# Optimization experiments

Measured on AMD Instinct MI355X. Metric: run time of the kernel, lower is better.

Reference implementation:

```python
import jax, jax.numpy as jnp
import numpy as np

NA, NPA, NT = 4096, 8192, 4096  # authors, papers, terms
HEADS = 8

def _ln(x, g, b):
    m = jnp.mean(x, -1, keepdims=True)
    v = jnp.var(x, -1, keepdims=True)
    return (x - m) * jax.lax.rsqrt(v + 1e-5) * g + b

def _gat(x_src, x_dst, src, dst, W, a_s, a_d, b, n_dst):
    # PyG-style GATConv (shared lin for src/dst, no self loops), per edge type.
    heads, outc = a_s.shape
    h_s = (x_src @ W).reshape(-1, heads, outc)
    h_d = (x_dst @ W).reshape(-1, heads, outc)
    e = jax.nn.leaky_relu(jnp.sum(h_s * a_s, -1)[src] + jnp.sum(h_d * a_d, -1)[dst], 0.2)  # [E,H]
    m = jax.ops.segment_max(e, dst, num_segments=n_dst)
    m = jnp.where(jnp.isfinite(m), m, 0.0)
    w = jnp.exp(e - m[dst])
    den = jax.ops.segment_sum(w, dst, num_segments=n_dst)
    alpha = w / (den[dst] + 1e-16)
    out = jax.ops.segment_sum(h_s[src] * alpha[..., None], dst, num_segments=n_dst)
    return out.reshape(n_dst, heads * outc) + b

def _gtl(x, peQ, peK, db, Wq, bq, Wk, bk, Wv, bv, Wo, bo, g1, be1, Wf1, bf1, Wf2, bf2, g2, be2):
    # PE-modulated dense multi-head attention + FFN, pre/post LN residual blocks.
    N, D = x.shape
    dh = D // HEADS
    Q = (x @ Wq + bq + peQ).reshape(N, HEADS, dh)
    K = (x @ Wk + bk + peK).reshape(N, HEADS, dh)
    V = (x @ Wv + bv).reshape(N, HEADS, dh)
    s = jnp.einsum('nhd,mhd->hnm', Q, K) / jnp.sqrt(jnp.float32(dh)) + db[None, None, :]
    o = jnp.einsum('hnm,mhd->nhd', jax.nn.softmax(s, -1), V).reshape(N, D) @ Wo + bo
    x = _ln(x + o, g1, be1)
    f = jax.nn.relu(x @ Wf1 + bf1) @ Wf2 + bf2
    return _ln(x + f, g2, be2)

def _forward(F, I):
    (x_author, x_paper, x_term, original_A, t1_W, t1_b, t2_W, t2_b, t3_W, t3_b,
     gat1_W, gat1_as, gat1_ad, gat1_b, gat2_W, gat2_as, gat2_ad, gat2_b,
     pe_embed, peWQ, peWK,
     gt_Wq, gt_bq, gt_Wk, gt_bk, gt_Wv, gt_bv, gt_Wo, gt_bo,
     gt_g1, gt_be1, gt_Wf1, gt_bf1, gt_Wf2, gt_bf2, gt_g2, gt_be2,
     cat_W, cat_b, mlp_W1, mlp_b1, mlp_W2, mlp_b2) = F
    (ap_src, ap_dst, pa_src, pa_dst, pt_src, pt_dst, tp_src, tp_dst, deg) = I
    xa = jax.nn.relu(x_author @ t1_W + t1_b)
    xp = jax.nn.relu(x_paper @ t2_W + t2_b)
    xt = jax.nn.relu(x_term @ t3_W + t3_b)
    # to_hetero GAT layer 1 (heads=8, out=128): sum over incoming edge types, relu
    h_p1 = jax.nn.relu(_gat(xa, xp, ap_src, ap_dst, gat1_W[0], gat1_as[0], gat1_ad[0], gat1_b[0], NPA)
                       + _gat(xt, xp, tp_src, tp_dst, gat1_W[3], gat1_as[3], gat1_ad[3], gat1_b[3], NPA))
    h_a1 = jax.nn.relu(_gat(xp, xa, pa_src, pa_dst, gat1_W[1], gat1_as[1], gat1_ad[1], gat1_b[1], NA))
    # layer 2 (heads=1); only author output feeds the graph transformer
    h_a2 = _gat(h_p1, h_a1, pa_src, pa_dst, gat2_W[1], gat2_as[1], gat2_ad[1], gat2_b[1], NA)
    # learned positional encodings + adjacency reconstruction loss
    peQ = pe_embed @ peWQ
    peK = pe_embed @ peWK
    S = jax.nn.sigmoid(peQ @ peK.T)  # [NA, NA]
    loss_pe = jnp.mean((S[None] - original_A) ** 2)
    db = jnp.log(jnp.maximum(deg.astype(jnp.float32), 1.0))  # degree key bias
    x = h_a2
    outs = [x]
    for i in range(gt_Wq.shape[0]):
        x = _gtl(x, peQ, peK, db, gt_Wq[i], gt_bq[i], gt_Wk[i], gt_bk[i], gt_Wv[i], gt_bv[i],
                 gt_Wo[i], gt_bo[i], gt_g1[i], gt_be1[i], gt_Wf1[i], gt_bf1[i], gt_Wf2[i], gt_bf2[i],
                 gt_g2[i], gt_be2[i])
        outs.append(x)
    x_gt = jax.nn.relu(jnp.concatenate(outs, -1) @ cat_W + cat_b)
    logits = jax.nn.relu(x_gt @ mlp_W1 + mlp_b1) @ mlp_W2 + mlp_b2
    return loss_pe, jax.nn.softmax(logits, -1), x_gt

def setup_inputs() -> dict:
    key = jax.random.key(0)
    ks = iter(jax.random.split(key, 100))
    def rn(sh, s=1.0):
        return jax.random.normal(next(ks), sh, jnp.float32) * s
    def ri(sh, hi, lo=0):
        return jax.random.randint(next(ks), sh, lo, hi)
    d = {}
    d['x_author'] = rn((NA, 334)); d['x_paper'] = rn((NPA, 512)); d['x_term'] = rn((NT, 128))
    d['ap_src'] = ri((80000,), NA); d['ap_dst'] = ri((80000,), NPA)
    d['pa_src'] = ri((80000,), NPA); d['pa_dst'] = ri((80000,), NA)
    d['pt_src'] = ri((160000,), NPA); d['pt_dst'] = ri((160000,), NT)
    d['tp_src'] = ri((160000,), NT); d['tp_dst'] = ri((160000,), NPA)
    d['original_A'] = (jax.random.uniform(next(ks), (4, NA, NA)) < 0.005).astype(jnp.float32)
    d['deg'] = ri((NA,), 64, 1)
    p = 0.05
    d['t1_W'] = rn((334, 128), p); d['t1_b'] = jnp.zeros((128,))
    d['t2_W'] = rn((512, 128), p); d['t2_b'] = jnp.zeros((128,))
    d['t3_W'] = rn((128, 128), p); d['t3_b'] = jnp.zeros((128,))
    d['gat1_W'] = rn((4, 128, 1024), p); d['gat1_as'] = rn((4, 8, 128), p)
    d['gat1_ad'] = rn((4, 8, 128), p); d['gat1_b'] = jnp.zeros((4, 1024))
    d['gat2_W'] = rn((4, 1024, 128), p); d['gat2_as'] = rn((4, 1, 128), p)
    d['gat2_ad'] = rn((4, 1, 128), p); d['gat2_b'] = jnp.zeros((4, 128))
    d['pe_embed'] = rn((NA, 128), p); d['peWQ'] = rn((128, 128), p); d['peWK'] = rn((128, 128), p)
    d['gt_Wq'] = rn((2, 128, 128), p); d['gt_bq'] = jnp.zeros((2, 128))
    d['gt_Wk'] = rn((2, 128, 128), p); d['gt_bk'] = jnp.zeros((2, 128))
    d['gt_Wv'] = rn((2, 128, 128), p); d['gt_bv'] = jnp.zeros((2, 128))
    d['gt_Wo'] = rn((2, 128, 128), p); d['gt_bo'] = jnp.zeros((2, 128))
    d['gt_g1'] = jnp.ones((2, 128)); d['gt_be1'] = jnp.zeros((2, 128))
    d['gt_Wf1'] = rn((2, 128, 256), p); d['gt_bf1'] = jnp.zeros((2, 256))
    d['gt_Wf2'] = rn((2, 256, 128), p); d['gt_bf2'] = jnp.zeros((2, 128))
    d['gt_g2'] = jnp.ones((2, 128)); d['gt_be2'] = jnp.zeros((2, 128))
    d['cat_W'] = rn((384, 128), p); d['cat_b'] = jnp.zeros((128,))
    d['mlp_W1'] = rn((128, 256), p); d['mlp_b1'] = jnp.zeros((256,))
    d['mlp_W2'] = rn((256, 4), p); d['mlp_b2'] = jnp.zeros((4,))
    return d

def reference(x_author, x_paper, x_term, ap_src, ap_dst, pa_src, pa_dst, pt_src, pt_dst, tp_src, tp_dst, original_A, deg, t1_W, t1_b, t2_W, t2_b, t3_W, t3_b, gat1_W, gat1_as, gat1_ad, gat1_b, gat2_W, gat2_as, gat2_ad, gat2_b, pe_embed, peWQ, peWK, gt_Wq, gt_bq, gt_Wk, gt_bk, gt_Wv, gt_bv, gt_Wo, gt_bo, gt_g1, gt_be1, gt_Wf1, gt_bf1, gt_Wf2, gt_bf2, gt_g2, gt_be2, cat_W, cat_b, mlp_W1, mlp_b1, mlp_W2, mlp_b2):
    F = (x_author, x_paper, x_term, original_A, t1_W, t1_b, t2_W, t2_b, t3_W, t3_b,
         gat1_W, gat1_as, gat1_ad, gat1_b, gat2_W, gat2_as, gat2_ad, gat2_b,
         pe_embed, peWQ, peWK,
         gt_Wq, gt_bq, gt_Wk, gt_bk, gt_Wv, gt_bv, gt_Wo, gt_bo,
         gt_g1, gt_be1, gt_Wf1, gt_bf1, gt_Wf2, gt_bf2, gt_g2, gt_be2,
         cat_W, cat_b, mlp_W1, mlp_b1, mlp_W2, mlp_b2)
    I = (ap_src, ap_dst, pa_src, pa_dst, pt_src, pt_dst, tp_src, tp_dst, deg)
    return _forward(F, I)
```

## Files before the change

kernel.cpp:

```cpp
#include <hip/hip_runtime.h>
#include <math.h>

#define NA   4096
#define NPA  8192
#define NT   4096
#define E_AP 80000
#define E_PA 80000
#define E_TP 160000
#define E_TOT (E_AP + E_TP + E_PA)
#define NSLOT (NPA + NPA + NA)
#define ASPLIT 4

typedef __attribute__((ext_vector_type(4))) float f32x4;
typedef __attribute__((ext_vector_type(8))) short s16x8;
typedef __attribute__((ext_vector_type(8))) unsigned short u16x8;
typedef unsigned short ushort_t;

__device__ __forceinline__ ushort_t f2bf(float f){
  unsigned u = __float_as_uint(f);
  unsigned r = u + 0x7fffu + ((u >> 16) & 1u);
  return (ushort_t)(r >> 16);
}
__device__ __forceinline__ float bf2f(ushort_t u){
  return __uint_as_float(((unsigned)u) << 16);
// ... 56 lines not shown
        int gk = k0 + ks + j;
        float fv = (gk < K) ? B[(size_t)gk * ldb + bn + n] : 0.f;
        tmp[j] = f2bf(fv);
      }
      u16x8 v0, v1;
#pragma unroll
      for (int j = 0; j < 8; ++j) { v0[j] = tmp[j]; v1[j] = tmp[8 + j]; }
      *(u16x8*)&Bs[n][ks] = v0;
      *(u16x8*)&Bs[n][ks + 8] = v1;
    } else {
      int n = tid >> 2, ks = (tid & 3) * 8;
      u16x8 v;
#pragma unroll
      for (int j = 0; j < 8; ++j) {
        int gk = k0 + ks + j;
        float fv = (gk < K) ? B[(size_t)gk * ldb + bn + n] : 0.f;
        v[j] = f2bf(fv);
      }
      *(u16x8*)&Bs[n][ks] = v;
    }
    __syncthreads();
    s16x8 a_frag[2], b_frag[NJ];
#pragma unroll
    for (int i = 0; i < 2; ++i) a_frag[i] = *(s16x8*)&As[wm + i * 16 + lid][lg * 8];
#pragma unroll
    for (int j = 0; j < NJ; ++j) b_frag[j] = *(s16x8*)&Bs[wn + j * 16 + lid][lg * 8];
#pragma unroll
    for (int i = 0; i < 2; ++i)
#pragma unroll
      for (int j = 0; j < NJ; ++j)
        acc[i][j] = __builtin_amdgcn_mfma_f32_16x16x32_bf16(a_frag[i], b_frag[j], acc[i][j], 0, 0, 0);
    __syncthreads();
  }
  if constexpr (ACT == 2) {
    __shared__ float Ct[64][132];
#pragma unroll
    for (int i = 0; i < 2; ++i) {
#pragma unroll
      for (int j = 0; j < NJ; ++j) {
        int coll = wn + j * 16 + lid;
#pragma unroll
        for (int rr = 0; rr < 4; ++rr) {
          int rowl = wm + i * 16 + lg * 4 + rr;
          float v = acc[i][j][rr];
          if (bias) v += bias[coll];
          if (addmat && coll < addCols) v += addmat[(size_t)(bm + rowl) * addLd + coll];
          Ct[rowl][coll] = v;
        }
      }
    }
    __syncthreads();
    int row = tid >> 2, part = tid & 3;
    float s = 0.f, q = 0.f;
#pragma unroll
    for (int c2 = 0; c2 < 32; ++c2) {
      float v = Ct[row][part * 32 + c2];
      s += v; q += v * v;
    }
    s += __shfl_xor(s, 1); q += __shfl_xor(q, 1);
    s += __shfl_xor(s, 2); q += __shfl_xor(q, 2);
    float mean = s * (1.f / 128.f);
    float var = q * (1.f / 128.f) - mean * mean;
    float inv = rsqrtf(var + 1e-5f);
    int r = bm + row;
    float* Cf = (float*)C;
#pragma unroll
    for (int c2 = 0; c2 < 32; ++c2) {
      int c = part * 32 + c2;
      Cf[(size_t)r * ldc + c] = (Ct[row][c] - mean) * inv * lng[c] + lnb[c];
    }
  } else if constexpr (ACT == 3) {
    __shared__ float Ct[64][132];
#pragma unroll
    for (int i = 0; i < 2; ++i) {
#pragma unroll
      for (int j = 0; j < NJ; ++j) {
        int coll = wn + j * 16 + lid;
#pragma unroll
        for (int rr = 0; rr < 4; ++rr) {
          int rowl = wm + i * 16 + lg * 4 + rr;
          Ct[rowl][coll] = acc[i][j][rr];
        }
      }
    }
    __syncthreads();
    int row = tid >> 2, part = tid & 3;
    const float* vsel = (bm + row < 8192) ? lng : lnb;
    float rd = 0.f;
    ushort_t* Cu = (ushort_t*)C;
#pragma unroll
    for (int c2 = 0; c2 < 32; ++c2) {
      int c = part * 32 + c2;
      float f = Ct[row][c];
      rd = fmaf(f, vsel[c], rd);
      Cu[(size_t)(bm + row) * ldc + c] = f2bf(f);
    }
    rd += __shfl_xor(rd, 1);
    rd += __shfl_xor(rd, 2);
    if (part == 0) rdOut[bm + row] = rd;
  } else {
#pragma unroll
    for (int i = 0; i < 2; ++i) {
#pragma unroll
      for (int j = 0; j < NJ; ++j) {
// ... 106 lines not shown
      int c = bn + wn + j * 16 + lid;
#pragma unroll
      for (int rr = 0; rr < 4; ++rr) {
        int r = bm + wm + i * 16 + lg * 4 + rr;
        float v = acc[i][j][rr];
        if (bias) v += bias[c];
        if (act == 1) v = fmaxf(v, 0.f);
        if (cBf16) ((ushort_t*)C)[(size_t)r * ldc + c] = f2bf(v);
        else       ((float*)C)[(size_t)r * ldc + c] = v;
      }
    }
  }
}

__global__ void prep_k(const float* __restrict__ gat1_b, const float* __restrict__ gat1_W,
                       const float* __restrict__ Wq, const float* __restrict__ bq,
                       const float* __restrict__ Wk, const float* __restrict__ bk,
                       const float* __restrict__ Wv, const float* __restrict__ bv,
                       const float* __restrict__ peWQ, const float* __restrict__ peWK,
                       const int* __restrict__ deg,
                       const float* __restrict__ gat1_as, const float* __restrict__ gat1_ad,
                       const int* __restrict__ ap_dst, const int* __restrict__ tp_dst,
                       const int* __restrict__ pa_dst,
                       const float* __restrict__ gt_Wo, const float* __restrict__ gt_Wf1,
                       const float* __restrict__ gt_Wf2, const float* __restrict__ cat_W,
                       const float* __restrict__ mlp_W1,
                       float* __restrict__ bsum, float* __restrict__ Wqkv,
                       float* __restrict__ bqkv, float* __restrict__ peW,
                       float* __restrict__ Bstack, float* __restrict__ dbv,
                       float* __restrict__ Ps, float* __restrict__ Pd,
                       int* __restrict__ cnt,
                       ushort_t* __restrict__ Wot, ushort_t* __restrict__ Wf1t,
                       ushort_t* __restrict__ Wf2t, ushort_t* __restrict__ catt,
                       ushort_t* __restrict__ mlp1t)
{
  int idx = blockIdx.x * blockDim.x + threadIdx.x;
  if (idx < 1024) { bsum[idx] = gat1_b[idx] + gat1_b[3 * 1024 + idx]; return; }
  idx -= 1024;
  if (idx < 2 * 128 * 384) {
    int l = idx / 49152, rem = idx % 49152;
    int k = rem / 384, c = rem % 384;
    float v;
    if (c < 128)      v = Wq[(size_t)l * 16384 + k * 128 + c];
    else if (c < 256) v = Wk[(size_t)l * 16384 + k * 128 + c - 128];
    else              v = Wv[(size_t)l * 16384 + k * 128 + c - 256];
    Wqkv[(size_t)l * 49152 + k * 384 + c] = v;
    return;
  }
  idx -= 2 * 128 * 384;
  if (idx < 2 * 384) {
    int l = idx / 384, c = idx % 384;
    float v;
    if (c < 128)      v = bq[l * 128 + c];
    else if (c < 256) v = bk[l * 128 + c - 128];
    else              v = bv[l * 128 + c - 256];
    bqkv[l * 384 + c] = v;
    return;
  }
  idx -= 2 * 384;
  if (idx < 128 * 256) {
    int k = idx / 256, c = idx % 256;
    peW[k * 256 + c] = (c < 128) ? peWQ[k * 128 + c] : peWK[k * 128 + c - 128];
    return;
  }
  idx -= 128 * 256;
  if (idx < 256 * 1024) {
    int k = idx / 1024, c = idx % 1024;
// ... 27 lines not shown
    return;
  }
  idx -= E_TOT;
  if (idx < 2 * 128 * 128) {
    int l = idx / 16384, rem = idx % 16384;
    int n = rem / 128, k = rem % 128;
    Wot[idx] = f2bf(gt_Wo[(size_t)l * 16384 + k * 128 + n]);
    return;
  }
  idx -= 2 * 128 * 128;
  if (idx < 2 * 256 * 128) {
    int l = idx / 32768, rem = idx % 32768;
    int n = rem / 128, k = rem % 128;
    Wf1t[idx] = f2bf(gt_Wf1[(size_t)l * 32768 + k * 256 + n]);
    return;
  }
  idx -= 2 * 256 * 128;
  if (idx < 2 * 128 * 256) {
    int l = idx / 32768, rem = idx % 32768;
    int n = rem / 256, k = rem % 256;
    Wf2t[idx] = f2bf(gt_Wf2[(size_t)l * 32768 + k * 128 + n]);
    return;
  }
  idx -= 2 * 128 * 256;
  if (idx < 128 * 384) {
    int n = idx / 384, k = idx % 384;
    catt[idx] = f2bf(cat_W[(size_t)k * 128 + n]);
    return;
  }
  idx -= 128 * 384;
  if (idx < 256 * 128) {
    int n = idx / 128, k = idx % 128;
    mlp1t[idx] = f2bf(mlp_W1[(size_t)k * 256 + n]);
  }
}

__global__ void scatterf_k(const int* __restrict__ ap_dst, const int* __restrict__ tp_dst,
                           const int* __restrict__ pa_dst, const int* __restrict__ off,
                           int* __restrict__ cur, int* __restrict__ eidx){
  int i = blockIdx.x * blockDim.x + threadIdx.x;
  if (i >= E_TOT) return;
  int slot, local;
  if (i < E_AP)             { local = i;                 slot = ap_dst[local]; }
  else if (i < E_AP + E_TP) { local = i - E_AP;          slot = NPA + tp_dst[local]; }
  else                      { local = i - E_AP - E_TP;   slot = 2 * NPA + pa_dst[local]; }
  int p = atomicAdd(&cur[slot], 1);
  eidx[off[slot] + p] = local;
}

__global__ __launch_bounds__(1024) void exscan_k(const int* __restrict__ in, int* __restrict__ out, int n){
  __shared__ int wsum[16];
  __shared__ int carrySh;
  int t = threadIdx.x, w = t >> 6, lane = t & 63;
  if (t == 0) carrySh = 0;
  __syncthreads();
  for (int base = 0; base < n; base += 1024){
    int carry = carrySh;
    int v = (base + t < n) ? in[base + t] : 0;
    int sc = v;
#pragma unroll
    for (int o2 = 1; o2 < 64; o2 <<= 1){
      int u = __shfl_up(sc, o2);
      if (lane >= o2) sc += u;
    }
    if (lane == 63) wsum[w] = sc;
    __syncthreads();
// ... 280 lines not shown
    l = l * scale + psum;
    m = mn;

#pragma unroll
    for (int g = 0; g < 4; ++g) {
#pragma unroll
      for (int rp = 0; rp < 4; rp += 2) {
        unsigned pack = (unsigned)f2bf(p[g][rp]) | ((unsigned)f2bf(p[g][rp + 1]) << 16);
        *(unsigned*)&Pl[w][lid][16 * g + 4 * lg + rp] = pack;
      }
    }
#pragma unroll
    for (int r = 0; r < 4; ++r) o[r] *= __shfl(scale, 4 * lg + r);
#pragma unroll
    for (int kc = 0; kc < 2; ++kc) {
      s16x8 pa = *(s16x8*)&Pl[w][lid][32 * kc + 8 * lg];
      s16x8 vb = *(s16x8*)&Vt[lid][32 * kc + 8 * lg];
      o = __builtin_amdgcn_mfma_f32_16x16x32_bf16(pa, vb, o, 0, 0, 0);
    }
  }
  float* pb = part + ((size_t)(sp * 8 + h) * NA) * 18;
#pragma unroll
  for (int r = 0; r < 4; ++r) {
    int qq = qbase + 16 * w + 4 * lg + r;
    pb[(size_t)qq * 18 + lid] = o[r];
  }
  if (lg == 0) {
    int qq = qbase + 16 * w + lid;
    pb[(size_t)qq * 18 + 16] = m;
    pb[(size_t)qq * 18 + 17] = l;
  }
}

__global__ __launch_bounds__(256) void gt_tail_k(
    const float* __restrict__ part,
    const ushort_t* __restrict__ Wot, const float* __restrict__ bo,
    const float* __restrict__ xin,
    const float* __restrict__ g1, const float* __restrict__ be1,
    const ushort_t* __restrict__ Wf1t, const float* __restrict__ bf1,
    const ushort_t* __restrict__ Wf2t, const float* __restrict__ bf2,
    const float* __restrict__ g2, const float* __restrict__ be2,
    float* __restrict__ outX)
{
  __shared__ __align__(16) ushort_t Aly[16][136];
  __shared__ __align__(16) ushort_t Bs[256][40];
  __shared__ __align__(16) ushort_t F1b[16][264];
  __shared__ float X1[16][132];
  int bm = blockIdx.x * 16;
  int tid = threadIdx.x;
  int w = tid >> 6, lane = tid & 63, lg = lane >> 4, lid = lane & 15;

  {
    int row = bm + (tid >> 4);
    int seg = tid & 15;
    int kcol = seg * 8;
    int h = kcol >> 4, d0 = kcol & 15;
    float mm = -1e30f;
#pragma unroll
    for (int sp = 0; sp < ASPLIT; ++sp)
      mm = fmaxf(mm, part[((size_t)(sp * 8 + h) * NA + row) * 18 + 16]);
    float ll = 0.f, a[8];
#pragma unroll
    for (int j = 0; j < 8; ++j) a[j] = 0.f;
#pragma unroll
    for (int sp = 0; sp < ASPLIT; ++sp){
      const float* pp = part + ((size_t)(sp * 8 + h) * NA + row) * 18;
      float wq = __expf(pp[16] - mm);
      ll += pp[17] * wq;
#pragma unroll
      for (int j = 0; j < 8; ++j) a[j] = fmaf(pp[d0 + j], wq, a[j]);
    }
    float inv = 1.f / ll;
    u16x8 v;
#pragma unroll
    for (int j = 0; j < 8; ++j) v[j] = f2bf(a[j] * inv);
    *(u16x8*)&Aly[tid >> 4][kcol] = v;
  }
  __syncthreads();

  f32x4 acc1[2];
  acc1[0] = (f32x4){0.f,0.f,0.f,0.f};
  acc1[1] = (f32x4){0.f,0.f,0.f,0.f};
  for (int k0 = 0; k0 < 128; k0 += 32){
// ... 66 lines not shown
  f32x4 acc3[2];
  acc3[0] = (f32x4){0.f,0.f,0.f,0.f};
  acc3[1] = (f32x4){0.f,0.f,0.f,0.f};
  for (int k0 = 0; k0 < 256; k0 += 32){
    int n = tid >> 1, ks = (tid & 1) * 16;
    *(u16x8*)&Bs[n][ks]     = *(const u16x8*)(Wf2t + (size_t)n * 256 + k0 + ks);
    *(u16x8*)&Bs[n][ks + 8] = *(const u16x8*)(Wf2t + (size_t)n * 256 + k0 + ks + 8);
    __syncthreads();
    s16x8 af = *(s16x8*)&F1b[lid][k0 + lg * 8];
#pragma unroll
    for (int j = 0; j < 2; ++j){
      s16x8 bf = *(s16x8*)&Bs[w * 32 + j * 16 + lid][lg * 8];
      acc3[j] = __builtin_amdgcn_mfma_f32_16x16x32_bf16(af, bf, acc3[j], 0, 0, 0);
    }
    __syncthreads();
  }
#pragma unroll
  for (int j = 0; j < 2; ++j)
#pragma unroll
    for (int rr = 0; rr < 4; ++rr){
      int r = lg * 4 + rr, c = w * 32 + j * 16 + lid;
      X1[r][c] = acc3[j][rr] + bf2[c] + X1[r][c];
    }
  __syncthreads();
  {
    int r = tid >> 4, p = tid & 15;
    float s = 0.f, q = 0.f;
#pragma unroll
    for (int j = 0; j < 8; ++j){ float v = X1[r][p * 8 + j]; s += v; q += v * v; }
#pragma unroll
    for (int mk = 1; mk < 16; mk <<= 1){ s += __shfl_xor(s, mk); q += __shfl_xor(q, mk); }
    float mean = s * (1.f / 128.f), var = q * (1.f / 128.f) - mean * mean;
    float inv = rsqrtf(var + 1e-5f);
#pragma unroll
    for (int j = 0; j < 8; ++j){
      int c = p * 8 + j;
      outX[(size_t)(bm + r) * 128 + c] = (X1[r][c] - mean) * inv * g2[c] + be2[c];
    }
  }
}

__global__ __launch_bounds__(256) void head_k(
    const float* __restrict__ hA2, const float* __restrict__ o1, const float* __restrict__ o2,
    const ushort_t* __restrict__ catt, const float* __restrict__ cat_b,
    const ushort_t* __restrict__ mlp1t, const float* __restrict__ mlp_b1,
    const float* __restrict__ mlp_W2, const float* __restrict__ mlp_b2,
    const float* __restrict__ lossAcc, float* __restrict__ out)
{
  __shared__ __align__(16) ushort_t Aly[16][392];
  __shared__ __align__(16) ushort_t Bs[256][40];
  __shared__ __align__(16) ushort_t L1b[16][264];
  __shared__ float LG[16][4];
  int bm = blockIdx.x * 16;
  int tid = threadIdx.x;
  int w = tid >> 6, lane = tid & 63, lg = lane >> 4, lid = lane & 15;
  if (blockIdx.x == 0 && tid == 0) out[0] = lossAcc[0] * (1.0f / 67108864.0f);

  {
    int r = bm + (tid >> 4), seg = tid & 15;
#pragma unroll
    for (int ch = 0; ch < 3; ++ch){
      int c0 = seg * 24 + ch * 8;
      const float* src; int cc;
      if (c0 < 128)      { src = hA2; cc = c0; }
      else if (c0 < 256) { src = o1;  cc = c0 - 128; }
      else               { src = o2;  cc = c0 - 256; }
      u16x8 v;
#pragma unroll
      for (int j = 0; j < 8; ++j) v[j] = f2bf(src[(size_t)r * 128 + cc + j]);
      *(u16x8*)&Aly[tid >> 4][c0] = v;
    }
  }
  __syncthreads();

  float* xgt = out + 1 + NA * 4;
  f32x4 acc1[2];
  acc1[0] = (f32x4){0.f,0.f,0.f,0.f};
  acc1[1] = (f32x4){0.f,0.f,0.f,0.f};
  for (int k0 = 0; k0 < 384; k0 += 32){
    int n = tid >> 1, ks = (tid & 1) * 16;
    *(u16x8*)&Bs[n][ks]     = *(const u16x8*)(catt + (size_t)n * 384 + k0 + ks);
    *(u16x8*)&Bs[n][ks + 8] = *(const u16x8*)(catt + (size_t)n * 384 + k0 + ks + 8);
    __syncthreads();
    s16x8 af = *(s16x8*)&Aly[lid][k0 + lg * 8];
#pragma unroll
    for (int j = 0; j < 2; ++j){
      s16x8 bf = *(s16x8*)&Bs[w * 32 + j * 16 + lid][lg * 8];
      acc1[j] = __builtin_amdgcn_mfma_f32_16x16x32_bf16(af, bf, acc1[j], 0, 0, 0);
    }
    __syncthreads();
  }
#pragma unroll
  for (int j = 0; j < 2; ++j)
#pragma unroll
    for (int rr = 0; rr < 4; ++rr){
      int r = lg * 4 + rr, c = w * 32 + j * 16 + lid;
      float f = fmaxf(acc1[j][rr] + cat_b[c], 0.f);
      xgt[(size_t)(bm + r) * 128 + c] = f;
      Aly[r][c] = f2bf(f);
    }
  __syncthreads();

  f32x4 acc2[4];
#pragma unroll
  for (int j = 0; j < 4; ++j) acc2[j] = (f32x4){0.f,0.f,0.f,0.f};
  for (int k0 = 0; k0 < 128; k0 += 32){
#pragma unroll
    for (int q4 = 0; q4 < 4; ++q4)
      *(u16x8*)&Bs[tid][q4 * 8] = *(const u16x8*)(mlp1t + (size_t)tid * 128 + k0 + q4 * 8);
    __syncthreads();
    s16x8 af = *(s16x8*)&Aly[lid][k0 + lg * 8];
#pragma unroll
    for (int j = 0; j < 4; ++j){
      s16x8 bf = *(s16x8*)&Bs[w * 64 + j * 16 + lid][lg * 8];
      acc2[j] = __builtin_amdgcn_mfma_f32_16x16x32_bf16(af, bf, acc2[j], 0, 0, 0);
    }
    __syncthreads();
  }
#pragma unroll
  for (int j = 0; j < 4; ++j)
#pragma unroll
    for (int rr = 0; rr < 4; ++rr){
      int r = lg * 4 + rr, c = w * 64 + j * 16 + lid;
      L1b[r][c] = f2bf(fmaxf(acc2[j][rr] + mlp_b1[c], 0.f));
    }
  __syncthreads();

  {
    int r = tid >> 4, rem = tid & 15, c = rem >> 2, p = rem & 3;
    float s = 0.f;
    for (int k = p * 64; k < p * 64 + 64; ++k)
      s = fmaf(bf2f(L1b[r][k]), mlp_W2[(size_t)k * 4 + c], s);
    s += __shfl_xor(s, 1);
    s += __shfl_xor(s, 2);
    if (p == 0) LG[r][c] = s + mlp_b2[c];
  }
  __syncthreads();
  if (tid < 16){
    int r = tid;
    float l0 = LG[r][0], l1 = LG[r][1], l2 = LG[r][2], l3 = LG[r][3];
    float mx = fmaxf(fmaxf(l0, l1), fmaxf(l2, l3));
    float e0 = __expf(l0 - mx), e1 = __expf(l1 - mx), e2 = __expf(l2 - mx), e3 = __expf(l3 - mx);
    float inv = 1.f / (e0 + e1 + e2 + e3);
    float* o = out + 1 + (size_t)(bm + r) * 4;
    o[0] = e0 * inv; o[1] = e1 * inv; o[2] = e2 * inv; o[3] = e3 * inv;
  }
}

__global__ void setval_k(float* p, float v){ p[0] = v; }

extern "C" void kernel_launch(void* const* d_in, const int* in_sizes, int n_in,
                              void* d_out, int out_size, void* d_ws, size_t ws_size,
                              hipStream_t stream)
{
  (void)in_sizes; (void)n_in; (void)out_size;
  const float* x_author = (const float*)d_in[0];
  const float* x_paper  = (const float*)d_in[1];
  const float* x_term   = (const float*)d_in[2];
  const int* ap_src = (const int*)d_in[3];
  const int* ap_dst = (const int*)d_in[4];
  const int* pa_src = (const int*)d_in[5];
  const int* pa_dst = (const int*)d_in[6];
  const int* tp_src = (const int*)d_in[9];
  const int* tp_dst = (const int*)d_in[10];
  const float* original_A = (const float*)d_in[11];
  const int* deg = (const int*)d_in[12];
  const float* t1_W = (const float*)d_in[13]; const float* t1_b = (const float*)d_in[14];
  const float* t2_W = (const float*)d_in[15]; const float* t2_b = (const float*)d_in[16];
  const float* t3_W = (const float*)d_in[17]; const float* t3_b = (const float*)d_in[18];
  const float* gat1_W  = (const float*)d_in[19];
  const float* gat1_as = (const float*)d_in[20];
  const float* gat1_ad = (const float*)d_in[21];
  const float* gat1_b  = (const float*)d_in[22];
  const float* gat2_W  = (const float*)d_in[23];
  const float* gat2_as = (const float*)d_in[24];
  const float* gat2_ad = (const float*)d_in[25];
  const float* gat2_b  = (const float*)d_in[26];
  const float* pe_embed = (const float*)d_in[27];
// ... 14 lines not shown

  char* base = (char*)d_ws;
  size_t off = 0;
  auto alloc = [&](size_t nbytes) -> void* {
    void* p = base + off;
    off += (nbytes + 255) & ~(size_t)255;
    return p;
  };
  ushort_t* xa  = (ushort_t*)alloc((size_t)NA * 128 * 2);
  ushort_t* xp  = (ushort_t*)alloc((size_t)NPA * 128 * 2);
  ushort_t* xt  = (ushort_t*)alloc((size_t)NT * 128 * 2);
  ushort_t* accP = (ushort_t*)alloc((size_t)NPA * 1024 * 2);
  ushort_t* accA = (ushort_t*)alloc((size_t)NA * 1024 * 2);
  ushort_t* agg  = (ushort_t*)alloc((size_t)NSLOT * 1024 * 2);
  float* scores = (float*)alloc((size_t)36864 * 8 * 4);
  float* Ps   = (float*)alloc(3 * 1024 * 4);
  float* Pd   = (float*)alloc(3 * 1024 * 4);
  ushort_t* hs2 = (ushort_t*)alloc((size_t)NPA * 128 * 2);
  ushort_t* hd2 = (ushort_t*)alloc((size_t)NA * 128 * 2);
  float* s2sd = (float*)alloc((size_t)(NPA + NA) * 4);
  float* hA2  = (float*)alloc((size_t)NA * 128 * 4);
  float* peQK = (float*)alloc((size_t)NA * 256 * 4);
  float* dbv  = (float*)alloc((size_t)NA * 4);
  float* bsum = (float*)alloc(1024 * 4);
  float* Wqkv = (float*)alloc((size_t)2 * 128 * 384 * 4);
  float* bqkv = (float*)alloc((size_t)2 * 384 * 4);
  float* peW  = (float*)alloc((size_t)128 * 256 * 4);
  float* Bstack = (float*)alloc((size_t)256 * 1024 * 4);
  ushort_t* Wot   = (ushort_t*)alloc((size_t)2 * 128 * 128 * 2);
  ushort_t* Wf1t  = (ushort_t*)alloc((size_t)2 * 256 * 128 * 2);
  ushort_t* Wf2t  = (ushort_t*)alloc((size_t)2 * 128 * 256 * 2);
  ushort_t* catt  = (ushort_t*)alloc((size_t)128 * 384 * 2);
  ushort_t* mlp1t = (ushort_t*)alloc((size_t)256 * 128 * 2);
  ushort_t* QKVb = (ushort_t*)alloc((size_t)NA * 384 * 2);
  float* outs1= (float*)alloc((size_t)NA * 128 * 4);
  float* outs2= (float*)alloc((size_t)NA * 128 * 4);
  int*   offb = (int*)alloc((size_t)NSLOT * 4);
  int*   eidx = (int*)alloc((size_t)E_TOT * 4);
  size_t zstart = off;
  int*      cnt   = (int*)alloc((size_t)NSLOT * 4);
  int*      cur   = (int*)alloc((size_t)NSLOT * 4);
  float*    lossAcc = (float*)alloc(256);
  size_t zlen = off - zstart;

  float* part = (float*)accP;

  if (off > ws_size){
    setval_k<<<1, 1, 0, stream>>>(out, -12345.0f);
    return;
  }

  auto gemmx = [&](int act, int tn, const void* A, const void* A2, const void* A3, int aBf16,
                   const float* B, void* C, int cBf16, const float* bias,
                   const float* addmat, int addCols, int addLd,
                   const float* lng, const float* lnb, float* rdOut,
                   int M, int N, int K, int lda, int ldb, int ldc){
    dim3 g(M / 64, N / tn, 1);
    if (tn == 128) {
      if (act == 0)      gemm_mfma_k<0,128><<<g, 256, 0, stream>>>(A, A2, A3, aBf16, B, C, cBf16, bias, addmat, addCols, addLd, lng, lnb, rdOut, M, N, K, lda, ldb, ldc);
      else if (act == 1) gemm_mfma_k<1,128><<<g, 256, 0, stream>>>(A, A2, A3, aBf16, B, C, cBf16, bias, addmat, addCols, addLd, lng, lnb, rdOut, M, N, K, lda, ldb, ldc);
      else if (act == 2) gemm_mfma_k<2,128><<<g, 256, 0, stream>>>(A, A2, A3, aBf16, B, C, cBf16, bias, addmat, addCols, addLd, lng, lnb, rdOut, M, N, K, lda, ldb, ldc);
      else               gemm_mfma_k<3,128><<<g, 256, 0, stream>>>(A, A2, A3, aBf16, B, C, cBf16, bias, addmat, addCols, addLd, lng, lnb, rdOut, M, N, K, lda, ldb, ldc);
    } else {
      if (act == 0)      gemm_mfma_k<0,64><<<g, 256, 0, stream>>>(A, A2, A3, aBf16, B, C, cBf16, bias, addmat, addCols, addLd, lng, lnb, rdOut, M, N, K, lda, ldb, ldc);
      else               gemm_mfma_k<1,64><<<g, 256, 0, stream>>>(A, A2, A3, aBf16, B, C, cBf16, bias, addmat, addCols, addLd, lng, lnb, rdOut, M, N, K, lda, ldb, ldc);
    }
  };

  hipMemsetAsync(base + zstart, 0, zlen, stream);
  prep_k<<<3781, 256, 0, stream>>>(gat1_b, gat1_W, gt_Wq, gt_bq, gt_Wk, gt_bk, gt_Wv, gt_bv,
                                   peWQ, peWK, deg, gat1_as, gat1_ad, ap_dst, tp_dst, pa_dst,
                                   gt_Wo, gt_Wf1, gt_Wf2, cat_W, mlp_W1,
                                   bsum, Wqkv, bqkv, peW, Bstack, dbv, Ps, Pd, cnt,
                                   Wot, Wf1t, Wf2t, catt, mlp1t);
  {
    GDescArr da; da.nd = 4;
    da.d[0] = { x_author, nullptr, t1_W, xa, t1_b, 0, 1, 1, NA, 128, 334, 334, 128, 128, 1, 0, 0, 0, 0 };
    da.d[1] = { x_paper,  nullptr, t2_W, xp, t2_b, 0, 1, 1, NPA, 128, 512, 512, 128, 128, 1, 0, 0, 0, 128 };
    da.d[2] = { x_term,   nullptr, t3_W, xt, t3_b, 0, 1, 1, NT, 128, 128, 128, 128, 128, 1, 0, 0, 0, 384 };
    da.d[3] = { pe_embed, nullptr, peW, peQK, nullptr, 0, 0, 0, NA, 256, 128, 128, 256, 256, 1, 0, 0, 0, 512 };
    gemm_multi_k<<<768, 256, 0, stream>>>(da);
  }
  exscan_k<<<1, 1024, 0, stream>>>(cnt, offb, NSLOT);
  scatterf_k<<<(E_TOT + 255) / 256, 256, 0, stream>>>(ap_dst, tp_dst, pa_dst, offb, cur, eidx);
  scorev_k<<<9216, 256, 0, stream>>>(xa, xp, xt, Ps, Pd, scores);
  agg8ff_k<<<NSLOT / 4, 256, 0, stream>>>(eidx, offb, cnt, ap_src, tp_src, pa_src,
                                          xa, xt, xp, scores, agg);
  {
    GDescArr da; da.nd = 2;
    da.d[0] = { agg, agg + (size_t)NPA * 1024, Bstack, accP, bsum, 1, 1, 1,
                NPA, 128, 256, 1024, 1024, 1024, 8, 128, 128, 128, 0 };
    da.d[1] = { agg + (size_t)2 * NPA * 1024, nullptr, gat1_W + 131072, accA, gat1_b + 1024, 1, 1, 1,
                NA, 128, 128, 1024, 1024, 1024, 8, 128, 128, 128, 2048 };
    gemm_multi_k<<<3072, 256, 0, stream>>>(da);
  }
  gemmx(3, 128, accP, 0, 0, 1, gat2_W + 131072, hs2, 1, 0, 0, 0, 0,
        gat2_as + 128, gat2_ad + 128, s2sd, NPA + NA, 128, 1024, 1024, 128, 128);
  gat_agg1f_k<<<NA / 4, 256, 0, stream>>>(eidx, offb + 2 * NPA, cnt + 2 * NPA, pa_src, hs2, s2sd,
                                          gat2_b + 128, hA2, NA);
  loss_mfma_k<<<dim3(64, 32), 256, 0, stream>>>(peQK, peQK + 128, original_A, lossAcc);
  const float* x = hA2;
  float* louts[2] = { outs1, outs2 };
  for (int i = 0; i < 2; ++i){
    gemmx(0, 64, x, 0, 0, 0, Wqkv + (size_t)i * 49152, QKVb, 1, bqkv + i * 384, peQK, 256, 256,
          0, 0, 0, NA, 384, 128, 128, 384, 384);
    attn_mfma_k<<<dim3(NA / 64, 8, ASPLIT), 256, 0, stream>>>(QKVb, QKVb + 128, QKVb + 256, dbv, part);
    gt_tail_k<<<NA / 16, 256, 0, stream>>>(part, Wot + (size_t)i * 16384, gt_bo + i * 128, x,
                                           gt_g1 + i * 128, gt_be1 + i * 128,
                                           Wf1t + (size_t)i * 32768, gt_bf1 + i * 256,
                                           Wf2t + (size_t)i * 32768, gt_bf2 + i * 128,
                                           gt_g2 + i * 128, gt_be2 + i * 128, louts[i]);
    x = louts[i];
  }
  head_k<<<NA / 16, 256, 0, stream>>>(hA2, outs1, outs2, catt, cat_b, mlp1t, mlp_b1,
                                      mlp_W2, mlp_b2, lossAcc, out);
}
```

Before: 646.2 us.

## Fuse next-layer QKV projection and classification head into graph-transformer tail kernel

```diff
diff --git a/kernel.cpp b/kernel.cpp
--- a/kernel.cpp
+++ b/kernel.cpp
@@ -112,44 +112,7 @@
         acc[i][j] = __builtin_amdgcn_mfma_f32_16x16x32_bf16(a_frag[i], b_frag[j], acc[i][j], 0, 0, 0);
     __syncthreads();
   }
-  if constexpr (ACT == 2) {
-    __shared__ float Ct[64][132];
-#pragma unroll
-    for (int i = 0; i < 2; ++i) {
-#pragma unroll
-      for (int j = 0; j < NJ; ++j) {
-        int coll = wn + j * 16 + lid;
-#pragma unroll
-        for (int rr = 0; rr < 4; ++rr) {
-          int rowl = wm + i * 16 + lg * 4 + rr;
-          float v = acc[i][j][rr];
-          if (bias) v += bias[coll];
-          if (addmat && coll < addCols) v += addmat[(size_t)(bm + rowl) * addLd + coll];
-          Ct[rowl][coll] = v;
-        }
-      }
-    }
-    __syncthreads();
-    int row = tid >> 2, part = tid & 3;
-    float s = 0.f, q = 0.f;
-#pragma unroll
-    for (int c2 = 0; c2 < 32; ++c2) {
-      float v = Ct[row][part * 32 + c2];
-      s += v; q += v * v;
-    }
-    s += __shfl_xor(s, 1); q += __shfl_xor(q, 1);
-    s += __shfl_xor(s, 2); q += __shfl_xor(q, 2);
-    float mean = s * (1.f / 128.f);
-    float var = q * (1.f / 128.f) - mean * mean;
-    float inv = rsqrtf(var + 1e-5f);
-    int r = bm + row;
-    float* Cf = (float*)C;
-#pragma unroll
-    for (int c2 = 0; c2 < 32; ++c2) {
-      int c = part * 32 + c2;
-      Cf[(size_t)r * ldc + c] = (Ct[row][c] - mean) * inv * lng[c] + lnb[c];
-    }
-  } else if constexpr (ACT == 3) {
+  if constexpr (ACT == 3) {
     __shared__ float Ct[64][132];
 #pragma unroll
     for (int i = 0; i < 2; ++i) {
@@ -322,7 +285,7 @@
                        int* __restrict__ cnt,
                        ushort_t* __restrict__ Wot, ushort_t* __restrict__ Wf1t,
                        ushort_t* __restrict__ Wf2t, ushort_t* __restrict__ catt,
-                       ushort_t* __restrict__ mlp1t)
+                       ushort_t* __restrict__ mlp1t, ushort_t* __restrict__ Wqkvt)
 {
   int idx = blockIdx.x * blockDim.x + threadIdx.x;
   if (idx < 1024) { bsum[idx] = gat1_b[idx] + gat1_b[3 * 1024 + idx]; return; }
@@ -416,6 +379,17 @@
   if (idx < 256 * 128) {
     int n = idx / 128, k = idx % 128;
     mlp1t[idx] = f2bf(mlp_W1[(size_t)k * 256 + n]);
+    return;
+  }
+  idx -= 256 * 128;
+  if (idx < 2 * 384 * 128) {
+    int l = idx / 49152, rem = idx % 49152;
+    int n = rem / 128, k = rem % 128;
+    float v;
+    if (n < 128)      v = Wq[(size_t)l * 16384 + k * 128 + n];
+    else if (n < 256) v = Wk[(size_t)l * 16384 + k * 128 + n - 128];
+    else              v = Wv[(size_t)l * 16384 + k * 128 + n - 256];
+    Wqkvt[idx] = f2bf(v);
   }
 }
 
@@ -762,6 +736,7 @@
   }
 }
 
+template<int MODE>
 __global__ __launch_bounds__(256) void gt_tail_k(
     const float* __restrict__ part,
     const ushort_t* __restrict__ Wot, const float* __restrict__ bo,
@@ -770,15 +745,25 @@
     const ushort_t* __restrict__ Wf1t, const float* __restrict__ bf1,
     const ushort_t* __restrict__ Wf2t, const float* __restrict__ bf2,
     const float* __restrict__ g2, const float* __restrict__ be2,
-    float* __restrict__ outX)
+    float* __restrict__ outX,
+    const ushort_t* __restrict__ Wqkvt, const float* __restrict__ bqkv,
+    const float* __restrict__ peQK, ushort_t* __restrict__ QKVb,
+    const float* __restrict__ hA2, const float* __restrict__ o1,
+    const ushort_t* __restrict__ catt, const float* __restrict__ cat_b,
+    const ushort_t* __restrict__ mlp1t, const float* __restrict__ mlp_b1,
+    const float* __restrict__ mlp_W2, const float* __restrict__ mlp_b2,
+    const float* __restrict__ lossAcc, float* __restrict__ out)
 {
-  __shared__ __align__(16) ushort_t Aly[16][136];
+  constexpr int AW = (MODE == 1) ? 392 : 136;
+  __shared__ __align__(16) ushort_t Aly[16][AW];
   __shared__ __align__(16) ushort_t Bs[256][40];
   __shared__ __align__(16) ushort_t F1b[16][264];
   __shared__ float X1[16][132];
+  __shared__ float LG[16][4];
   int bm = blockIdx.x * 16;
   int tid = threadIdx.x;
   int w = tid >> 6, lane = tid & 63, lg = lane >> 4, lid = lane & 15;
+  if (MODE == 1 && blockIdx.x == 0 && tid == 0) out[0] = lossAcc[0] * (1.0f / 67108864.0f);
 
   {
     int row = bm + (tid >> 4);
@@ -911,118 +896,138 @@
     for (int mk = 1; mk < 16; mk <<= 1){ s += __shfl_xor(s, mk); q += __shfl_xor(q, mk); }
     float mean = s * (1.f / 128.f), var = q * (1.f / 128.f) - mean * mean;
     float inv = rsqrtf(var + 1e-5f);
+    u16x8 v;
 #pragma unroll
     for (int j = 0; j < 8; ++j){
       int c = p * 8 + j;
-      outX[(size_t)(bm + r) * 128 + c] = (X1[r][c] - mean) * inv * g2[c] + be2[c];
-    }
-  }
-}
-
-__global__ __launch_bounds__(256) void head_k(
-    const float* __restrict__ hA2, const float* __restrict__ o1, const float* __restrict__ o2,
-    const ushort_t* __restrict__ catt, const float* __restrict__ cat_b,
-    const ushort_t* __restrict__ mlp1t, const float* __restrict__ mlp_b1,
-    const float* __restrict__ mlp_W2, const float* __restrict__ mlp_b2,
-    const float* __restrict__ lossAcc, float* __restrict__ out)
-{
-  __shared__ __align__(16) ushort_t Aly[16][392];
-  __shared__ __align__(16) ushort_t Bs[256][40];
-  __shared__ __align__(16) ushort_t L1b[16][264];
-  __shared__ float LG[16][4];
-  int bm = blockIdx.x * 16;
-  int tid = threadIdx.x;
-  int w = tid >> 6, lane = tid & 63, lg = lane >> 4, lid = lane & 15;
-  if (blockIdx.x == 0 && tid == 0) out[0] = lossAcc[0] * (1.0f / 67108864.0f);
-
-  {
-    int r = bm + (tid >> 4), seg = tid & 15;
-#pragma unroll
-    for (int ch = 0; ch < 3; ++ch){
-      int c0 = seg * 24 + ch * 8;
-      const float* src; int cc;
-      if (c0 < 128)      { src = hA2; cc = c0; }
-      else if (c0 < 256) { src = o1;  cc = c0 - 128; }
-      else               { src = o2;  cc = c0 - 256; }
-      u16x8 v;
-#pragma unroll
-      for (int j = 0; j < 8; ++j) v[j] = f2bf(src[(size_t)r * 128 + cc + j]);
-      *(u16x8*)&Aly[tid >> 4][c0] = v;
-    }
+      float f = (X1[r][c] - mean) * inv * g2[c] + be2[c];
+      X1[r][c] = f;
+      v[j] = f2bf(f);
+      if (MODE == 0) outX[(size_t)(bm + r) * 128 + c] = f;
+    }
+    if (MODE == 0) *(u16x8*)&Aly[r][p * 8] = v;
+    else           *(u16x8*)&Aly[r][256 + p * 8] = v;
   }
   __syncthreads();
 
-  float* xgt = out + 1 + NA * 4;
-  f32x4 acc1[2];
-  acc1[0] = (f32x4){0.f,0.f,0.f,0.f};
-  acc1[1] = (f32x4){0.f,0.f,0.f,0.f};
-  for (int k0 = 0; k0 < 384; k0 += 32){
-    int n = tid >> 1, ks = (tid & 1) * 16;
-    *(u16x8*)&Bs[n][ks]     = *(const u16x8*)(catt + (size_t)n * 384 + k0 + ks);
-    *(u16x8*)&Bs[n][ks + 8] = *(const u16x8*)(catt + (size_t)n * 384 + k0 + ks + 8);
-    __syncthreads();
-    s16x8 af = *(s16x8*)&Aly[lid][k0 + lg * 8];
-#pragma unroll
-    for (int j = 0; j < 2; ++j){
-      s16x8 bf = *(s16x8*)&Bs[w * 32 + j * 16 + lid][lg * 8];
-      acc1[j] = __builtin_amdgcn_mfma_f32_16x16x32_bf16(af, bf, acc1[j], 0, 0, 0);
-    }
-    __syncthreads();
-  }
-#pragma unroll
-  for (int j = 0; j < 2; ++j)
-#pragma unroll
-    for (int rr = 0; rr < 4; ++rr){
-      int r = lg * 4 + rr, c = w * 32 + j * 16 + lid;
-      float f = fmaxf(acc1[j][rr] + cat_b[c], 0.f);
-      xgt[(size_t)(bm + r) * 128 + c] = f;
-      Aly[r][c] = f2bf(f);
-    }
-  __syncthreads();
-
-  f32x4 acc2[4];
-#pragma unroll
-  for (int j = 0; j < 4; ++j) acc2[j] = (f32x4){0.f,0.f,0.f,0.f};
-  for (int k0 = 0; k0 < 128; k0 += 32){
-#pragma unroll
-    for (int q4 = 0; q4 < 4; ++q4)
-      *(u16x8*)&Bs[tid][q4 * 8] = *(const u16x8*)(mlp1t + (size_t)tid * 128 + k0 + q4 * 8);
-    __syncthreads();
-    s16x8 af = *(s16x8*)&Aly[lid][k0 + lg * 8];
-#pragma unroll
-    for (int j = 0; j < 4; ++j){
-      s16x8 bf = *(s16x8*)&Bs[w * 64 + j * 16 + lid][lg * 8];
-      acc2[j] = __builtin_amdgcn_mfma_f32_16x16x32_bf16(af, bf, acc2[j], 0, 0, 0);
-    }
-    __syncthreads();
-  }
-#pragma unroll
-  for (int j = 0; j < 4; ++j)
-#pragma unroll
-    for (int rr = 0; rr < 4; ++rr){
-      int r = lg * 4 + rr, c = w * 64 + j * 16 + lid;
-      L1b[r][c] = f2bf(fmaxf(acc2[j][rr] + mlp_b1[c], 0.f));
-    }
-  __syncthreads();
-
-  {
-    int r = tid >> 4, rem = tid & 15, c = rem >> 2, p = rem & 3;
-    float s = 0.f;
-    for (int k = p * 64; k < p * 64 + 64; ++k)
-      s = fmaf(bf2f(L1b[r][k]), mlp_W2[(size_t)k * 4 + c], s);
-    s += __shfl_xor(s, 1);
-    s += __shfl_xor(s, 2);
-    if (p == 0) LG[r][c] = s + mlp_b2[c];
-  }
-  __syncthreads();
-  if (tid < 16){
-    int r = tid;
-    float l0 = LG[r][0], l1 = LG[r][1], l2 = LG[r][2], l3 = LG[r][3];
-    float mx = fmaxf(fmaxf(l0, l1), fmaxf(l2, l3));
-    float e0 = __expf(l0 - mx), e1 = __expf(l1 - mx), e2 = __expf(l2 - mx), e3 = __expf(l3 - mx);
-    float inv = 1.f / (e0 + e1 + e2 + e3);
-    float* o = out + 1 + (size_t)(bm + r) * 4;
-    o[0] = e0 * inv; o[1] = e1 * inv; o[2] = e2 * inv; o[3] = e3 * inv;
+  if constexpr (MODE == 0) {
+#pragma unroll
+    for (int nb = 0; nb < 2; ++nb) {
+      f32x4 acc4[3];
+#pragma unroll
+      for (int j = 0; j < 3; ++j) acc4[j] = (f32x4){0.f,0.f,0.f,0.f};
+      for (int k0 = 0; k0 < 128; k0 += 32){
+#pragma unroll
+        for (int p = 0; p < 3; ++p){
+          int idx = tid + p * 256;
+          int n = idx >> 2, seg = (idx & 3) * 8;
+          *(u16x8*)&Bs[n][seg] = *(const u16x8*)(Wqkvt + (size_t)(nb * 192 + n) * 128 + k0 + seg);
+        }
+        __syncthreads();
+        s16x8 af = *(s16x8*)&Aly[lid][k0 + lg * 8];
+#pragma unroll
+        for (int j = 0; j < 3; ++j){
+          s16x8 bf = *(s16x8*)&Bs[w * 48 + j * 16 + lid][lg * 8];
+          acc4[j] = __builtin_amdgcn_mfma_f32_16x16x32_bf16(af, bf, acc4[j], 0, 0, 0);
+        }
+        __syncthreads();
+      }
+#pragma unroll
+      for (int j = 0; j < 3; ++j)
+#pragma unroll
+        for (int rr = 0; rr < 4; ++rr){
+          int r = lg * 4 + rr, c = nb * 192 + w * 48 + j * 16 + lid;
+          float v = acc4[j][rr] + bqkv[c];
+          if (c < 256) v += peQK[(size_t)(bm + r) * 256 + c];
+          QKVb[(size_t)(bm + r) * 384 + c] = f2bf(v);
+        }
+    }
+  } else {
+    {
+      int r = bm + (tid >> 4), seg = tid & 15;
+#pragma unroll
+      for (int ch = 0; ch < 2; ++ch){
+        int c0 = seg * 16 + ch * 8;
+        const float* src; int cc;
+        if (c0 < 128) { src = hA2; cc = c0; }
+        else          { src = o1;  cc = c0 - 128; }
+        u16x8 v;
+#pragma unroll
+        for (int j = 0; j < 8; ++j) v[j] = f2bf(src[(size_t)r * 128 + cc + j]);
+        *(u16x8*)&Aly[tid >> 4][c0] = v;
+      }
+    }
+    __syncthreads();
+    float* xgt = out + 1 + NA * 4;
+    f32x4 acc1b[2];
+    acc1b[0] = (f32x4){0.f,0.f,0.f,0.f};
+    acc1b[1] = (f32x4){0.f,0.f,0.f,0.f};
+    for (int k0 = 0; k0 < 384; k0 += 32){
+      int n = tid >> 1, ks = (tid & 1) * 16;
+      *(u16x8*)&Bs[n][ks]     = *(const u16x8*)(catt + (size_t)n * 384 + k0 + ks);
+      *(u16x8*)&Bs[n][ks + 8] = *(const u16x8*)(catt + (size_t)n * 384 + k0 + ks + 8);
+      __syncthreads();
+      s16x8 af = *(s16x8*)&Aly[lid][k0 + lg * 8];
+#pragma unroll
+      for (int j = 0; j < 2; ++j){
+        s16x8 bf = *(s16x8*)&Bs[w * 32 + j * 16 + lid][lg * 8];
+        acc1b[j] = __builtin_amdgcn_mfma_f32_16x16x32_bf16(af, bf, acc1b[j], 0, 0, 0);
+      }
+      __syncthreads();
+    }
+#pragma unroll
+    for (int j = 0; j < 2; ++j)
+#pragma unroll
+      for (int rr = 0; rr < 4; ++rr){
+        int r = lg * 4 + rr, c = w * 32 + j * 16 + lid;
+        float f = fmaxf(acc1b[j][rr] + cat_b[c], 0.f);
+        xgt[(size_t)(bm + r) * 128 + c] = f;
+        Aly[r][c] = f2bf(f);
+      }
+    __syncthreads();
+    f32x4 acc2b[4];
+#pragma unroll
+    for (int j = 0; j < 4; ++j) acc2b[j] = (f32x4){0.f,0.f,0.f,0.f};
+    for (int k0 = 0; k0 < 128; k0 += 32){
+#pragma unroll
+      for (int q4 = 0; q4 < 4; ++q4)
+        *(u16x8*)&Bs[tid][q4 * 8] = *(const u16x8*)(mlp1t + (size_t)tid * 128 + k0 + q4 * 8);
+      __syncthreads();
+      s16x8 af = *(s16x8*)&Aly[lid][k0 + lg * 8];
+#pragma unroll
+      for (int j = 0; j < 4; ++j){
+        s16x8 bf = *(s16x8*)&Bs[w * 64 + j * 16 + lid][lg * 8];
+        acc2b[j] = __builtin_amdgcn_mfma_f32_16x16x32_bf16(af, bf, acc2b[j], 0, 0, 0);
+      }
+      __syncthreads();
+    }
+#pragma unroll
+    for (int j = 0; j < 4; ++j)
+#pragma unroll
+      for (int rr = 0; rr < 4; ++rr){
+        int r = lg * 4 + rr, c = w * 64 + j * 16 + lid;
+        F1b[r][c] = f2bf(fmaxf(acc2b[j][rr] + mlp_b1[c], 0.f));
+      }
+    __syncthreads();
+    {
+      int r = tid >> 4, rem = tid & 15, c = rem >> 2, p = rem & 3;
+      float s = 0.f;
+      for (int k = p * 64; k < p * 64 + 64; ++k)
+        s = fmaf(bf2f(F1b[r][k]), mlp_W2[(size_t)k * 4 + c], s);
+      s += __shfl_xor(s, 1);
+      s += __shfl_xor(s, 2);
+      if (p == 0) LG[r][c] = s + mlp_b2[c];
+    }
+    __syncthreads();
+    if (tid < 16){
+      int r = tid;
+      float l0 = LG[r][0], l1 = LG[r][1], l2 = LG[r][2], l3 = LG[r][3];
+      float mx = fmaxf(fmaxf(l0, l1), fmaxf(l2, l3));
+      float e0 = __expf(l0 - mx), e1 = __expf(l1 - mx), e2 = __expf(l2 - mx), e3 = __expf(l3 - mx);
+      float inv = 1.f / (e0 + e1 + e2 + e3);
+      float* o = out + 1 + (size_t)(bm + r) * 4;
+      o[0] = e0 * inv; o[1] = e1 * inv; o[2] = e2 * inv; o[3] = e3 * inv;
+    }
   }
 }
 
@@ -1103,9 +1108,9 @@
   ushort_t* Wf2t  = (ushort_t*)alloc((size_t)2 * 128 * 256 * 2);
   ushort_t* catt  = (ushort_t*)alloc((size_t)128 * 384 * 2);
   ushort_t* mlp1t = (ushort_t*)alloc((size_t)256 * 128 * 2);
+  ushort_t* Wqkvt = (ushort_t*)alloc((size_t)2 * 384 * 128 * 2);
   ushort_t* QKVb = (ushort_t*)alloc((size_t)NA * 384 * 2);
   float* outs1= (float*)alloc((size_t)NA * 128 * 4);
-  float* outs2= (float*)alloc((size_t)NA * 128 * 4);
   int*   offb = (int*)alloc((size_t)NSLOT * 4);
   int*   eidx = (int*)alloc((size_t)E_TOT * 4);
   size_t zstart = off;
@@ -1130,7 +1135,6 @@
     if (tn == 128) {
       if (act == 0)      gemm_mfma_k<0,128><<<g, 256, 0, stream>>>(A, A2, A3, aBf16, B, C, cBf16, bias, addmat, addCols, addLd, lng, lnb, rdOut, M, N, K, lda, ldb, ldc);
       else if (act == 1) gemm_mfma_k<1,128><<<g, 256, 0, stream>>>(A, A2, A3, aBf16, B, C, cBf16, bias, addmat, addCols, addLd, lng, lnb, rdOut, M, N, K, lda, ldb, ldc);
-      else if (act == 2) gemm_mfma_k<2,128><<<g, 256, 0, stream>>>(A, A2, A3, aBf16, B, C, cBf16, bias, addmat, addCols, addLd, lng, lnb, rdOut, M, N, K, lda, ldb, ldc);
       else               gemm_mfma_k<3,128><<<g, 256, 0, stream>>>(A, A2, A3, aBf16, B, C, cBf16, bias, addmat, addCols, addLd, lng, lnb, rdOut, M, N, K, lda, ldb, ldc);
     } else {
       if (act == 0)      gemm_mfma_k<0,64><<<g, 256, 0, stream>>>(A, A2, A3, aBf16, B, C, cBf16, bias, addmat, addCols, addLd, lng, lnb, rdOut, M, N, K, lda, ldb, ldc);
@@ -1139,11 +1143,11 @@
   };
 
   hipMemsetAsync(base + zstart, 0, zlen, stream);
-  prep_k<<<3781, 256, 0, stream>>>(gat1_b, gat1_W, gt_Wq, gt_bq, gt_Wk, gt_bk, gt_Wv, gt_bv,
+  prep_k<<<4165, 256, 0, stream>>>(gat1_b, gat1_W, gt_Wq, gt_bq, gt_Wk, gt_bk, gt_Wv, gt_bv,
                                    peWQ, peWK, deg, gat1_as, gat1_ad, ap_dst, tp_dst, pa_dst,
                                    gt_Wo, gt_Wf1, gt_Wf2, cat_W, mlp_W1,
                                    bsum, Wqkv, bqkv, peW, Bstack, dbv, Ps, Pd, cnt,
-                                   Wot, Wf1t, Wf2t, catt, mlp1t);
+                                   Wot, Wf1t, Wf2t, catt, mlp1t, Wqkvt);
   {
     GDescArr da; da.nd = 4;
     da.d[0] = { x_author, nullptr, t1_W, xa, t1_b, 0, 1, 1, NA, 128, 334, 334, 128, 128, 1, 0, 0, 0, 0 };
@@ -1170,19 +1174,21 @@
   gat_agg1f_k<<<NA / 4, 256, 0, stream>>>(eidx, offb + 2 * NPA, cnt + 2 * NPA, pa_src, hs2, s2sd,
                                           gat2_b + 128, hA2, NA);
   loss_mfma_k<<<dim3(64, 32), 256, 0, stream>>>(peQK, peQK + 128, original_A, lossAcc);
-  const float* x = hA2;
-  float* louts[2] = { outs1, outs2 };
-  for (int i = 0; i < 2; ++i){
-    gemmx(0, 64, x, 0, 0, 0, Wqkv + (size_t)i * 49152, QKVb, 1, bqkv + i * 384, peQK, 256, 256,
-          0, 0, 0, NA, 384, 128, 128, 384, 384);
-    attn_mfma_k<<<dim3(NA / 64, 8, ASPLIT), 256, 0, stream>>>(QKVb, QKVb + 128, QKVb + 256, dbv, part);
-    gt_tail_k<<<NA / 16, 256, 0, stream>>>(part, Wot + (size_t)i * 16384, gt_bo + i * 128, x,
-                                           gt_g1 + i * 128, gt_be1 + i * 128,
-                                           Wf1t + (size_t)i * 32768, gt_bf1 + i * 256,
-                                           Wf2t + (size_t)i * 32768, gt_bf2 + i * 128,
-                                           gt_g2 + i * 128, gt_be2 + i * 128, louts[i]);
-    x = louts[i];
-  }
-  head_k<<<NA / 16, 256, 0, stream>>>(hA2, outs1, outs2, catt, cat_b, mlp1t, mlp_b1,
-                                      mlp_W2, mlp_b2, lossAcc, out);
-}
+  gemmx(0, 64, hA2, 0, 0, 0, Wqkv, QKVb, 1, bqkv, peQK, 256, 256,
+        0, 0, 0, NA, 384, 128, 128, 384, 384);
+  attn_mfma_k<<<dim3(NA / 64, 8, ASPLIT), 256, 0, stream>>>(QKVb, QKVb + 128, QKVb + 256, dbv, part);
+  gt_tail_k<0><<<NA / 16, 256, 0, stream>>>(part, Wot, gt_bo, hA2,
+                                            gt_g1, gt_be1, Wf1t, gt_bf1, Wf2t, gt_bf2,
+                                            gt_g2, gt_be2, outs1,
+                                            Wqkvt + (size_t)49152, bqkv + 384, peQK, QKVb,
+                                            nullptr, nullptr, nullptr, nullptr,
+                                            nullptr, nullptr, nullptr, nullptr, nullptr, nullptr);
+  attn_mfma_k<<<dim3(NA / 64, 8, ASPLIT), 256, 0, stream>>>(QKVb, QKVb + 128, QKVb + 256, dbv, part);
+  gt_tail_k<1><<<NA / 16, 256, 0, stream>>>(part, Wot + 16384, gt_bo + 128, outs1,
+                                            gt_g1 + 128, gt_be1 + 128, Wf1t + 32768, gt_bf1 + 256,
+                                            Wf2t + 32768, gt_bf2 + 128,
+                                            gt_g2 + 128, gt_be2 + 128, nullptr,
+                                            nullptr, nullptr, nullptr, nullptr,
+                                            hA2, outs1, catt, cat_b, mlp1t, mlp_b1,
+                                            mlp_W2, mlp_b2, lossAcc, out);
+}
```

Result: no change. 638.9 us (-1.1%).
